# Kernel optimization log

Hardware: AMD Instinct MI355X
Metric: run time of the kernel (lower is better)

## Reference

```python
import jax, jax.numpy as jnp
import numpy as np

B, N, DX, E, H, HD, KH, FF = 8, 8192, 2, 128, 8, 16, 32, 128
G1, G2, PMAX = 32, 32, 32


def _ln(x, g, b):
    mu = jnp.mean(x, axis=-1, keepdims=True)
    var = jnp.mean((x - mu) ** 2, axis=-1, keepdims=True)
    return (x - mu) * jax.lax.rsqrt(var + 1e-5) * g + b


def _cumcount_row(idx):
    # for each element, number of earlier elements with the same value (stable)
    n = idx.shape[0]
    order = jnp.argsort(idx)  # stable
    si = idx[order]
    ar = jnp.arange(n)
    is_start = jnp.concatenate([jnp.ones((1,), bool), si[1:] != si[:-1]])
    seg_start = jax.lax.associative_scan(jnp.maximum, jnp.where(is_start, ar, 0))
    return jnp.zeros(n, jnp.int32).at[order].set((ar - seg_start).astype(jnp.int32))


def _forward(x, z, latent, Wq, Wk, Wv, Wo, bo, kW1, kb1, kW2, kb2,
             lnq_g, lnq_b, lnk_g, lnk_b, ln2_g, ln2_b, fW1, fb1, fW2, fb2,
             grid_n1, grid_n2, max_patch, num_heads):
    Bb, Nn, dx = x.shape
    e = latent.shape[0]
    dims = (grid_n1, grid_n2)
    M = grid_n1 * grid_n2
    P = max_patch
    h = num_heads
    hd = Wq.shape[1] // h
    # grid range from data (margin = 0), regular grid via linspace
    mins = [jnp.min(x[:, :, i]) for i in range(dx)]
    maxs = [jnp.max(x[:, :, i]) for i in range(dx)]
    axes = [jnp.linspace(mins[i], maxs[i], dims[i]) for i in range(dx)]
    x_grid = jnp.stack(jnp.meshgrid(*axes, indexing="ij"), axis=-1)  # [G1,G2,dx]
    x_grid_flat = x_grid.reshape(M, dx)
    # nearest grid cell per point: regular grid -> per-dim rounding
    flat = None
    for i in range(dx):
        step = (maxs[i] - mins[i]) / (dims[i] - 1)
        ii = jnp.clip(jnp.round((x[..., i] - mins[i]) / step), 0, dims[i] - 1).astype(jnp.int32)
        flat = ii if flat is None else flat * dims[i] + ii
    cell = flat  # [B,N]
    cumc = jax.vmap(_cumcount_row)(cell)          # slot within cell
    slot = jnp.where(cumc < P, cumc, P)           # overflow -> dummy slot (dropped)
    bidx = jnp.broadcast_to(jnp.arange(Bb)[:, None], (Bb, Nn))
    # scatter points into per-cell padded neighbour sets [B, M, P, d]
    jx = jnp.zeros((Bb, M, P + 1, dx), x.dtype).at[bidx, cell, slot].set(x)[:, :, :P]
    jz = jnp.zeros((Bb, M, P + 1, e), z.dtype).at[bidx, cell, slot].set(z)[:, :, :P]
    msk = jnp.zeros((Bb, M, P + 1), bool).at[bidx, cell, slot].set(True)[:, :, :P]
    xg = jnp.broadcast_to(x_grid_flat[None], (Bb, M, dx))
    zg = jnp.broadcast_to(latent[None, None, :], (Bb, M, e))
    # concatenate_x_grid=True: grid token prepended, always attended
    joint_x = jnp.concatenate([xg[:, :, None, :], jx], axis=2).reshape(Bb * M, P + 1, dx)
    joint_z = jnp.concatenate([zg[:, :, None, :], jz], axis=2).reshape(Bb * M, P + 1, e)
    att_mask = jnp.concatenate([jnp.ones((Bb, M, 1), bool), msk], axis=2).reshape(Bb * M, P + 1)
    xq = xg.reshape(Bb * M, 1, dx)
    zq = zg.reshape(Bb * M, 1, e)
    T = Bb * M
    # masked translation-equivariant cross-attention (pre-norm layer)
    q = jnp.einsum("tqe,ef->tqf", _ln(zq, lnq_g, lnq_b), Wq).reshape(T, 1, h, hd)
    zk_n = _ln(joint_z, lnk_g, lnk_b)
    k = jnp.einsum("tke,ef->tkf", zk_n, Wk).reshape(T, P + 1, h, hd)
    v = jnp.einsum("tke,ef->tkf", zk_n, Wv).reshape(T, P + 1, h, hd)
    dots = jnp.einsum("tqhd,tkhd->thqk", q, k) / jnp.sqrt(jnp.asarray(hd, q.dtype))
    diff = joint_x[:, None, :, :] - xq[:, :, None, :]            # [T,1,P+1,dx]
    kb = jnp.maximum(diff @ kW1 + kb1, 0.0) @ kW2 + kb2          # kernel bias [T,1,P+1,h]
    dots = dots + jnp.transpose(kb, (0, 3, 1, 2))
    dots = jnp.where(att_mask[:, None, None, :], dots, -1e9)
    A = jax.nn.softmax(dots, axis=-1)                            # [T,h,1,P+1]
    out = jnp.einsum("thqk,tkhd->tqhd", A, v).reshape(T, 1, h * hd)
    z_new = zq + out @ Wo + bo
    z_new = z_new + (jnp.maximum(_ln(z_new, ln2_g, ln2_b) @ fW1 + fb1, 0.0) @ fW2 + fb2)
    x_new = jnp.einsum("tqk,tkd->tqd", jnp.mean(A, axis=1), joint_x)  # TE location update
    x_grid_out = x_new.reshape(Bb, grid_n1, grid_n2, dx)
    z_grid_out = z_new.reshape(Bb, grid_n1, grid_n2, e)
    return (x_grid_out, z_grid_out)


def setup_inputs():
    key = jax.random.key(0)
    ks = jax.random.split(key, 12)
    s = 0.05
    return {
        "x": jax.random.uniform(ks[0], (B, N, DX), jnp.float32),
        "z": jax.random.normal(ks[1], (B, N, E), jnp.float32),
        "grid_n1": G1, "grid_n2": G2, "max_patch": PMAX, "num_heads": H,
        "latent": jax.random.normal(ks[2], (E,), jnp.float32),
        "Wq": jax.random.normal(ks[3], (E, H * HD), jnp.float32) * s,
        "Wk": jax.random.normal(ks[4], (E, H * HD), jnp.float32) * s,
        "Wv": jax.random.normal(ks[5], (E, H * HD), jnp.float32) * s,
        "Wo": jax.random.normal(ks[6], (H * HD, E), jnp.float32) * s,
        "bo": jnp.zeros((E,), jnp.float32),
        "kW1": jax.random.normal(ks[7], (DX, KH), jnp.float32) * s,
        "kb1": jnp.zeros((KH,), jnp.float32),
        "kW2": jax.random.normal(ks[8], (KH, H), jnp.float32) * s,
        "kb2": jnp.zeros((H,), jnp.float32),
        "lnq_g": jnp.ones((E,), jnp.float32), "lnq_b": jnp.zeros((E,), jnp.float32),
        "lnk_g": jnp.ones((E,), jnp.float32), "lnk_b": jnp.zeros((E,), jnp.float32),
        "ln2_g": jnp.ones((E,), jnp.float32), "ln2_b": jnp.zeros((E,), jnp.float32),
        "fW1": jax.random.normal(ks[9], (E, FF), jnp.float32) * s,
        "fb1": jnp.zeros((FF,), jnp.float32),
        "fW2": jax.random.normal(ks[10], (FF, E), jnp.float32) * s,
        "fb2": jnp.zeros((E,), jnp.float32),
    }


def reference(x, z, grid_n1, grid_n2, max_patch, num_heads, latent, Wq, Wk, Wv, Wo, bo,
              kW1, kb1, kW2, kb2, lnq_g, lnq_b, lnk_g, lnk_b, ln2_g, ln2_b,
              fW1, fb1, fW2, fb2):
    return _forward(x, z, latent, Wq, Wk, Wv, Wo, bo, kW1, kb1, kW2, kb2,
                    lnq_g, lnq_b, lnk_g, lnk_b, ln2_g, ln2_b, fW1, fb1, fW2, fb2,
                    grid_n1, grid_n2, max_patch, num_heads)
```

## Files before the change

### kernel.cpp

```cpp
#include <hip/hip_runtime.h>
#include <stdint.h>

#define NB 8
#define NN 8192
#define NE 128
#define NH 8
#define NHD 16
#define NKH 32
#define NFF 128
#define NG 32
#define NM 1024
#define NP 32
#define NT 8192
#define NPTS 65536

typedef __attribute__((ext_vector_type(8))) short bf16x8_t;
typedef __attribute__((ext_vector_type(4))) float f32x4_t;

#define WS_MM      0
#define WS_D0      64
#define WS_Q       128
#define WS_VG      640
#define WS_PART    1152
#define WS_CNT     2048
#define WS_CELL    34816
#define WS_PIDX    296960
#define WS_WKVT    1345536
#define WS_WOT     1411072
#define WS_FW1T    1443840
#define WS_FW2T    1476608
#define WS_KV      3606528

__device__ __forceinline__ unsigned short f2bf(float f) {
    unsigned u = __float_as_uint(f);
    u += 0x7FFFu + ((u >> 16) & 1u);
    return (unsigned short)(u >> 16);
}
__device__ __forceinline__ float bf2f(unsigned short h) {
    return __uint_as_float(((unsigned)h) << 16);
}
__device__ __forceinline__ float bflo(unsigned w) { return __uint_as_float(w << 16); }
__device__ __forceinline__ float bfhi(unsigned w) { return __uint_as_float(w & 0xFFFF0000u); }

__global__ __launch_bounds__(256) void k_setup(
        const float* __restrict__ x,
        const float* __restrict__ Wk, const float* __restrict__ Wv, const float* __restrict__ Wo,
        const float* __restrict__ fW1, const float* __restrict__ fW2,
        const float* __restrict__ latent, const float* __restrict__ Wq,
        const float* __restrict__ lnq_g, const float* __restrict__ lnq_b,
        const float* __restrict__ lnk_g, const float* __restrict__ lnk_b,
        const float* __restrict__ kb1, const float* __restrict__ kW2, const float* __restrict__ kb2,
        int* __restrict__ cnt,
        unsigned short* __restrict__ WkvT, unsigned short* __restrict__ WoT,
        unsigned short* __restrict__ fW1T, unsigned short* __restrict__ fW2T,
        float* __restrict__ ws_q, float* __restrict__ ws_vg, float* __restrict__ ws_d0,
        float4* __restrict__ part) {
    int blk = blockIdx.x;
    int t = threadIdx.x;
    if (blk < 20) {
        __shared__ float s_t[64][65];
        const float* src; unsigned short* dst;
        int n0, k0, srcN0;
        if (blk < 8) {
            int tn = blk >> 1, tk = blk & 1;
            n0 = tn * 64; k0 = tk * 64;
            dst = WkvT;
            if (n0 < 128) { src = Wk; srcN0 = n0; }
            else          { src = Wv; srcN0 = n0 - 128; }
        } else {
            int m = (blk - 8) >> 2, s4 = (blk - 8) & 3;
            int tn = s4 >> 1, tk = s4 & 1;
            n0 = tn * 64; k0 = tk * 64; srcN0 = n0;
            src = (m == 0) ? Wo : (m == 1) ? fW1 : fW2;
            dst = (m == 0) ? WoT : (m == 1) ? fW1T : fW2T;
        }
        int tx = t & 63, ty = t >> 6;
        #pragma unroll
        for (int r = 0; r < 16; ++r) {
            int kr = r * 4 + ty;
            s_t[kr][tx] = src[(k0 + kr) * 128 + srcN0 + tx];
        }
        __syncthreads();
        #pragma unroll
        for (int r = 0; r < 16; ++r) {
            int nr = r * 4 + ty;
            dst[(n0 + nr) * 128 + k0 + tx] = f2bf(s_t[tx][nr]);
        }
    } else if (blk < 52) {
        int idx = (blk - 20) * 256 + t;
        cnt[idx] = 0;
    } else if (blk == 52) {
        __shared__ float s_qn[128], s_kn[128], s_q[128], s_kg[128];
        __shared__ float s_mu, s_rstd;
        if (t < 64) {
            float v0 = latent[t], v1 = latent[t + 64];
            float s = v0 + v1;
            for (int m = 32; m > 0; m >>= 1) s += __shfl_xor(s, m);
            float mu = s * (1.0f / 128.0f);
            float d0 = v0 - mu, d1 = v1 - mu;
            float q = d0 * d0 + d1 * d1;
            for (int m = 32; m > 0; m >>= 1) q += __shfl_xor(q, m);
            if (t == 0) { s_mu = mu; s_rstd = rsqrtf(q * (1.0f / 128.0f) + 1e-5f); }
        }
        __syncthreads();
        if (t < 128) {
            float nv = (latent[t] - s_mu) * s_rstd;
            s_qn[t] = nv * lnq_g[t] + lnq_b[t];
            s_kn[t] = nv * lnk_g[t] + lnk_b[t];
        }
        __syncthreads();
        if (t < 128) {
            float aq = 0.f, ak = 0.f, av = 0.f;
            for (int e = 0; e < 128; ++e) {
                aq += s_qn[e] * Wq[e * 128 + t];
                ak += s_kn[e] * Wk[e * 128 + t];
                av += s_kn[e] * Wv[e * 128 + t];
            }
            s_q[t] = aq; s_kg[t] = ak;
            ws_q[t] = aq; ws_vg[t] = av;
        }
        __syncthreads();
        if (t < 8) {
            float acc = 0.f;
            for (int d = 0; d < 16; ++d) acc += s_q[t * 16 + d] * s_kg[t * 16 + d];
            float kb0 = kb2[t];
            for (int j = 0; j < 32; ++j) kb0 += fmaxf(kb1[j], 0.f) * kW2[j * 8 + t];
            ws_d0[t] = acc * 0.25f + kb0;
        }
    } else {
        __shared__ float s_red[4][4];
        int pb = blk - 53;
        const float4* xp = (const float4*)x + pb * 1024;
        float mn0 = 1e30f, mx0 = -1e30f, mn1 = 1e30f, mx1 = -1e30f;
        #pragma unroll
        for (int it = 0; it < 4; ++it) {
            float4 v = xp[it * 256 + t];
            mn0 = fminf(mn0, fminf(v.x, v.z)); mx0 = fmaxf(mx0, fmaxf(v.x, v.z));
            mn1 = fminf(mn1, fminf(v.y, v.w)); mx1 = fmaxf(mx1, fmaxf(v.y, v.w));
        }
        #pragma unroll
        for (int m = 32; m > 0; m >>= 1) {
            mn0 = fminf(mn0, __shfl_xor(mn0, m)); mx0 = fmaxf(mx0, __shfl_xor(mx0, m));
            mn1 = fminf(mn1, __shfl_xor(mn1, m)); mx1 = fmaxf(mx1, __shfl_xor(mx1, m));
        }
        int w = t >> 6;
        if ((t & 63) == 0) {
            s_red[w][0] = mn0; s_red[w][1] = mn1; s_red[w][2] = mx0; s_red[w][3] = mx1;
        }
        __syncthreads();
        if (t == 0) {
            float a0 = fminf(fminf(s_red[0][0], s_red[1][0]), fminf(s_red[2][0], s_red[3][0]));
            float a1 = fminf(fminf(s_red[0][1], s_red[1][1]), fminf(s_red[2][1], s_red[3][1]));
            float b0 = fmaxf(fmaxf(s_red[0][2], s_red[1][2]), fmaxf(s_red[2][2], s_red[3][2]));
            float b1 = fmaxf(fmaxf(s_red[0][3], s_red[1][3]), fmaxf(s_red[2][3], s_red[3][3]));
            part[pb] = make_float4(a0, a1, b0, b1);
        }
    }
}

__global__ __launch_bounds__(256) void k_binkv(
        const float* __restrict__ x, const float* __restrict__ z,
        const float4* __restrict__ part, float* __restrict__ mm,
        const float* __restrict__ lnk_g, const float* __restrict__ lnk_b,
        const unsigned short* __restrict__ WkvT, unsigned short* __restrict__ kv,
        int* __restrict__ cell, int* __restrict__ cnt, int* __restrict__ ptIdx) {
    int t = threadIdx.x;
    if (blockIdx.x >= 1024) {
        int l = t & 63;
        float mn0 = 1e30f, mn1 = 1e30f, mx0 = -1e30f, mx1 = -1e30f;
        if (l < 32) { float4 p = part[l]; mn0 = p.x; mn1 = p.y; mx0 = p.z; mx1 = p.w; }
        #pragma unroll
        for (int m = 32; m > 0; m >>= 1) {
            mn0 = fminf(mn0, __shfl_xor(mn0, m)); mx0 = fmaxf(mx0, __shfl_xor(mx0, m));
            mn1 = fminf(mn1, __shfl_xor(mn1, m)); mx1 = fmaxf(mx1, __shfl_xor(mx1, m));
        }
        if (blockIdx.x == 1024 && t == 0) {
            mm[0] = mn0; mm[1] = mn1; mm[2] = mx0; mm[3] = mx1;
        }
        int i = (blockIdx.x - 1024) * 256 + t;
        float st0 = (mx0 - mn0) / 31.0f, st1 = (mx1 - mn1) / 31.0f;
        float2 xv = ((const float2*)x)[i];
        int i0 = (int)rintf((xv.x - mn0) / st0); i0 = min(max(i0, 0), 31);
        int i1 = (int)rintf((xv.y - mn1) / st1); i1 = min(max(i1, 0), 31);
        int c = i0 * 32 + i1;
        cell[i] = c;
        int bb = i >> 13;
        int slot = atomicAdd(&cnt[bb * NM + c], 1);
        if (slot < NP) ptIdx[(bb * NM + c) * NP + slot] = i & (NN - 1);
        return;
    }
    __shared__ unsigned short s_zn[64][136];
    __shared__ unsigned short s_stage[4][16][68];
    int w = t >> 6, lane = t & 63;
    long base = (long)blockIdx.x * 64;
    int sub = lane >> 5;
    int lq = lane & 31;
    int mrow = lane & 15, quad = lane >> 4;

    bf16x8_t afrag[4][4];
    #pragma unroll
    for (int j = 0; j < 4; ++j) {
        int ft = w * 4 + j;
        const unsigned short* ap = WkvT + (ft * 16 + mrow) * 128 + quad * 8;
        #pragma unroll
        for (int kc = 0; kc < 4; ++kc)
            afrag[j][kc] = *(const bf16x8_t*)(ap + kc * 32);
    }

    float4 g4 = ((const float4*)lnk_g)[lq];
    float4 b4 = ((const float4*)lnk_b)[lq];
    float4 v[8];
    #pragma unroll
    for (int i = 0; i < 8; ++i) {
        int pl = w * 16 + i * 2 + sub;
        v[i] = ((const float4*)z)[(base + pl) * 32 + lq];
    }
    #pragma unroll
    for (int i = 0; i < 8; ++i) {
        int pl = w * 16 + i * 2 + sub;
        float sum = v[i].x + v[i].y + v[i].z + v[i].w;
        float ssq = v[i].x * v[i].x + v[i].y * v[i].y + v[i].z * v[i].z + v[i].w * v[i].w;
        #pragma unroll
        for (int m = 1; m < 32; m <<= 1) {
            sum += __shfl_xor(sum, m);
            ssq += __shfl_xor(ssq, m);
        }
        float mu = sum * (1.0f / 128.0f);
        float var = fmaxf(ssq * (1.0f / 128.0f) - mu * mu, 0.0f);
        float rstd = rsqrtf(var + 1e-5f);
        float n0 = (v[i].x - mu) * rstd * g4.x + b4.x;
        float n1 = (v[i].y - mu) * rstd * g4.y + b4.y;
        float n2 = (v[i].z - mu) * rstd * g4.z + b4.z;
        float n3 = (v[i].w - mu) * rstd * g4.w + b4.w;
        unsigned d0 = (unsigned)f2bf(n0) | ((unsigned)f2bf(n1) << 16);
        unsigned d1 = (unsigned)f2bf(n2) | ((unsigned)f2bf(n3) << 16);
        *(uint2*)&s_zn[pl][lq * 4] = make_uint2(d0, d1);
    }
    __syncthreads();

    #pragma unroll
    for (int tau = 0; tau < 4; ++tau) {
        bf16x8_t bfrag[4];
        #pragma unroll
        for (int kc = 0; kc < 4; ++kc)
            bfrag[kc] = *(const bf16x8_t*)&s_zn[tau * 16 + mrow][kc * 32 + quad * 8];
        #pragma unroll
        for (int j = 0; j < 4; ++j) {
            f32x4_t acc = {0.f, 0.f, 0.f, 0.f};
            #pragma unroll
            for (int kc = 0; kc < 4; ++kc)
                acc = __builtin_amdgcn_mfma_f32_16x16x32_bf16(afrag[j][kc], bfrag[kc], acc, 0, 0, 0);
            unsigned d0 = (unsigned)f2bf(acc[0]) | ((unsigned)f2bf(acc[1]) << 16);
            unsigned d1 = (unsigned)f2bf(acc[2]) | ((unsigned)f2bf(acc[3]) << 16);
            *(uint2*)&s_stage[w][mrow][j * 16 + quad * 4] = make_uint2(d0, d1);
        }
        int tok = lane >> 3, u = lane & 7;
        long tk0 = base + tau * 16;
        uint4 ra = *(const uint4*)&s_stage[w][tok][u * 8];
        *(uint4*)(kv + (tk0 + tok) * 256 + w * 64 + u * 8) = ra;
        uint4 rb = *(const uint4*)&s_stage[w][tok + 8][u * 8];
        *(uint4*)(kv + (tk0 + tok + 8) * 256 + w * 64 + u * 8) = rb;
    }
}

__global__ __launch_bounds__(256) void k_attn(const float* __restrict__ x,
        const int* __restrict__ cell, const int* __restrict__ cnt, int* __restrict__ ptIdx,
        const float* __restrict__ mm, const unsigned short* __restrict__ kv,
        const float* __restrict__ ws_q, const float* __restrict__ ws_vg,
        const float* __restrict__ ws_d0,
        const float* __restrict__ kW1, const float* __restrict__ kb1,
        const float* __restrict__ kW2, const float* __restrict__ kb2,
        const float* __restrict__ latent, const float* __restrict__ bo,
        const float* __restrict__ ln2_g, const float* __restrict__ ln2_b,
        const float* __restrict__ fb1, const float* __restrict__ fb2,
        const unsigned short* __restrict__ WoT, const unsigned short* __restrict__ fW1T,
        const unsigned short* __restrict__ fW2T,
        float* __restrict__ xout, float* __restrict__ zout) {
    __shared__ unsigned short s_a[16][136];
    __shared__ unsigned short s_a2[16][136];
    __shared__ float s_z[4][128];
    __shared__ float s_lat[128], s_g2[128], s_b2[128], s_fb1v[128], s_fb2v[128];
    int t = threadIdx.x;
    int l = t & 63;
    int w = t >> 6;
    if (t < 128) {
        s_lat[t] = latent[t] + bo[t];
        s_g2[t] = ln2_g[t]; s_b2[t] = ln2_b[t];
        s_fb1v[t] = fb1[t]; s_fb2v[t] = fb2[t];
    }
    int bm = blockIdx.x * 4 + w;
    int b = bm >> 10;
    int h = l >> 3, jp = l & 7;

    float mn0 = mm[0], mn1 = mm[1], mx0 = mm[2], mx1 = mm[3];
    int i0 = (bm & 1023) >> 5, i1 = bm & 31;
    float st0 = (mx0 - mn0) / 31.0f, st1 = (mx1 - mn1) / 31.0f;
    float xg0 = (i0 == 31) ? mx0 : mn0 + i0 * st0;
    float xg1 = (i1 == 31) ? mx1 : mn1 + i1 * st1;
    int craw = cnt[bm];
    int c = min(craw, NP);
    if (craw > NP) {
        int mycell = bm & 1023;
        const int* cb = cell + b * NN;
        int run = 0;
        for (int ch = 0; ch < NN / 64 && run < NP; ++ch) {
            int n = ch * 64 + l;
            bool match = (cb[n] == mycell);
            unsigned long long mask = __ballot(match);
            if (match) {
                int rank = run + __popcll(mask & ((1ull << l) - 1ull));
                if (rank < NP) ptIdx[bm * NP + rank] = n;
            }
            run += __popcll(mask);
        }
    }

    float q0 = ws_q[2 * l] * 0.25f, q1 = ws_q[2 * l + 1] * 0.25f;
    float vg0 = ws_vg[2 * l], vg1 = ws_vg[2 * l + 1];
    float ag = ws_d0[h];
    float kb2h = kb2[h];
    float w1a[4], w1b[4], b1v[4], w2v[4];
    #pragma unroll
    for (int m = 0; m < 4; ++m) {
        int j = jp + 8 * m;
        w1a[m] = kW1[j]; w1b[m] = kW1[32 + j]; b1v[m] = kb1[j]; w2v[m] = kW2[j * 8 + h];
    }

    int idxreg = 0; float x0r = 0.f, x1r = 0.f;
    if (l < c) {
        idxreg = ptIdx[bm * NP + l];
        float2 xv = ((const float2*)x)[(size_t)b * NN + idxreg];
        x0r = xv.x; x1r = xv.y;
    }

    unsigned vreg[NP];
    float areg[4];
    #pragma unroll
    for (int k = 0; k < NP; ++k) vreg[k] = 0u;
    areg[0] = areg[1] = areg[2] = areg[3] = -1e30f;

    #pragma unroll
    for (int key = 0; key < NP; ++key) {
        if (key < c) {
            int idxk = __shfl(idxreg, key);
            const unsigned* rowp = (const unsigned*)kv + ((size_t)(b * NN + idxk) << 7);
            unsigned kw = rowp[l];
            vreg[key] = rowp[64 + l];
            float d0 = __shfl(x0r, key) - xg0;
            float d1 = __shfl(x1r, key) - xg1;
            float part = q0 * bflo(kw) + q1 * bfhi(kw);
            #pragma unroll
            for (int m = 0; m < 4; ++m) {
                float hj = fmaf(d0, w1a[m], fmaf(d1, w1b[m], b1v[m]));
                hj = fmaxf(hj, 0.f);
                part = fmaf(hj, w2v[m], part);
            }
            part += __shfl_xor(part, 1);
            part += __shfl_xor(part, 2);
            part += __shfl_xor(part, 4);
            float score = part + kb2h;
            if (jp == (key & 7)) areg[key >> 3] = score;
        }
    }

    float mx = fmaxf(fmaxf(areg[0], areg[1]), fmaxf(areg[2], areg[3]));
    mx = fmaxf(mx, ag);
    mx = fmaxf(mx, __shfl_xor(mx, 1));
    mx = fmaxf(mx, __shfl_xor(mx, 2));
    mx = fmaxf(mx, __shfl_xor(mx, 4));
    float e0 = __expf(areg[0] - mx), e1 = __expf(areg[1] - mx);
    float e2 = __expf(areg[2] - mx), e3 = __expf(areg[3] - mx);
    float eg = __expf(ag - mx);
    float s = e0 + e1 + e2 + e3;
    s += __shfl_xor(s, 1);
    s += __shfl_xor(s, 2);
    s += __shfl_xor(s, 4);
    s += eg;
    float inv = 1.0f / s;

    float accA = eg * inv * vg0, accB = eg * inv * vg1;
    #pragma unroll
    for (int key = 0; key < NP; ++key) {
        if (key < c) {
            int src = (l & 56) | (key & 7);
            float em = (key >> 3) == 0 ? e0 : (key >> 3) == 1 ? e1 : (key >> 3) == 2 ? e2 : e3;
            float a = __shfl(em, src) * inv;
            unsigned vw = vreg[key];
            accA = fmaf(a, bflo(vw), accA);
            accB = fmaf(a, bfhi(vw), accB);
        }
    }
    unsigned ow = ((unsigned)f2bf(accB) << 16) | (unsigned)f2bf(accA);
    *(unsigned*)&s_a[w][2 * l] = ow;

    float s0 = e0 * inv, s1 = e1 * inv, s2 = e2 * inv, s3 = e3 * inv, sg = eg * inv;
    #pragma unroll
    for (int m = 8; m <= 32; m <<= 1) {
        s0 += __shfl_xor(s0, m); s1 += __shfl_xor(s1, m);
        s2 += __shfl_xor(s2, m); s3 += __shfl_xor(s3, m);
        sg += __shfl_xor(sg, m);
    }
    float px0 = 0.f, px1 = 0.f;
    {
        float xx0, xx1;
        xx0 = __shfl(x0r, jp);      xx1 = __shfl(x1r, jp);
        px0 = fmaf(s0, xx0, px0);   px1 = fmaf(s0, xx1, px1);
        xx0 = __shfl(x0r, jp + 8);  xx1 = __shfl(x1r, jp + 8);
        px0 = fmaf(s1, xx0, px0);   px1 = fmaf(s1, xx1, px1);
        xx0 = __shfl(x0r, jp + 16); xx1 = __shfl(x1r, jp + 16);
        px0 = fmaf(s2, xx0, px0);   px1 = fmaf(s2, xx1, px1);
        xx0 = __shfl(x0r, jp + 24); xx1 = __shfl(x1r, jp + 24);
        px0 = fmaf(s3, xx0, px0);   px1 = fmaf(s3, xx1, px1);
    }
    px0 += __shfl_xor(px0, 1); px1 += __shfl_xor(px1, 1);
    px0 += __shfl_xor(px0, 2); px1 += __shfl_xor(px1, 2);
    px0 += __shfl_xor(px0, 4); px1 += __shfl_xor(px1, 4);
    if (l == 0) {
        xout[bm * 2]     = (px0 + sg * xg0) * 0.125f;
        xout[bm * 2 + 1] = (px1 + sg * xg1) * 0.125f;
    }

    __syncthreads();
    int mrow = l & 15, quad = l >> 4;
    int base4 = blockIdx.x * 4;
    {
        bf16x8_t a[4];
        #pragma unroll
        for (int kc = 0; kc < 4; ++kc)
            a[kc] = *(const bf16x8_t*)&s_a[mrow][kc * 32 + quad * 8];
        #pragma unroll
        for (int cc = 0; cc < 2; ++cc) {
            int ct = w * 2 + cc;
            f32x4_t acc = {0.f, 0.f, 0.f, 0.f};
            const unsigned short* bp = WoT + (ct * 16 + mrow) * 128 + quad * 8;
            #pragma unroll
            for (int kc = 0; kc < 4; ++kc)
                acc = __builtin_amdgcn_mfma_f32_16x16x32_bf16(a[kc], *(const bf16x8_t*)(bp + kc * 32), acc, 0, 0, 0);
            if (quad == 0) {
                int f = ct * 16 + mrow;
                #pragma unroll
                for (int r = 0; r < 4; ++r) s_z[r][f] = acc[r] + s_lat[f];
            }
        }
    }
    __syncthreads();
    {
        float v0 = s_z[w][l], v1 = s_z[w][l + 64];
        float ssum = v0 + v1;
        #pragma unroll
        for (int m = 32; m > 0; m >>= 1) ssum += __shfl_xor(ssum, m);
        float mu = ssum * (1.0f / 128.0f);
        float d0 = v0 - mu, d1 = v1 - mu;
        float qq = d0 * d0 + d1 * d1;
        #pragma unroll
        for (int m = 32; m > 0; m >>= 1) qq += __shfl_xor(qq, m);
        float rstd = rsqrtf(qq * (1.0f / 128.0f) + 1e-5f);
        s_a2[w][l]      = f2bf(d0 * rstd * s_g2[l] + s_b2[l]);
        s_a2[w][l + 64] = f2bf(d1 * rstd * s_g2[l + 64] + s_b2[l + 64]);
    }
    __syncthreads();
    {
        bf16x8_t a[4];
        #pragma unroll
        for (int kc = 0; kc < 4; ++kc)
            a[kc] = *(const bf16x8_t*)&s_a2[mrow][kc * 32 + quad * 8];
        #pragma unroll
        for (int cc = 0; cc < 2; ++cc) {
            int ct = w * 2 + cc;
            f32x4_t acc = {0.f, 0.f, 0.f, 0.f};
            const unsigned short* bp = fW1T + (ct * 16 + mrow) * 128 + quad * 8;
            #pragma unroll
            for (int kc = 0; kc < 4; ++kc)
                acc = __builtin_amdgcn_mfma_f32_16x16x32_bf16(a[kc], *(const bf16x8_t*)(bp + kc * 32), acc, 0, 0, 0);
            if (quad == 0) {
                int f = ct * 16 + mrow;
                #pragma unroll
                for (int r = 0; r < 4; ++r)
                    s_a[r][f] = f2bf(fmaxf(acc[r] + s_fb1v[f], 0.f));
            }
        }
    }
    __syncthreads();
    {
        bf16x8_t a[4];
        #pragma unroll
        for (int kc = 0; kc < 4; ++kc)
            a[kc] = *(const bf16x8_t*)&s_a[mrow][kc * 32 + quad * 8];
        #pragma unroll
        for (int cc = 0; cc < 2; ++cc) {
            int ct = w * 2 + cc;
            f32x4_t acc = {0.f, 0.f, 0.f, 0.f};
            const unsigned short* bp = fW2T + (ct * 16 + mrow) * 128 + quad * 8;
            #pragma unroll
            for (int kc = 0; kc < 4; ++kc)
                acc = __builtin_amdgcn_mfma_f32_16x16x32_bf16(a[kc], *(const bf16x8_t*)(bp + kc * 32), acc, 0, 0, 0);
            if (quad == 0) {
                int f = ct * 16 + mrow;
                #pragma unroll
                for (int r = 0; r < 4; ++r)
                    zout[(base4 + r) * 128 + f] = s_z[r][f] + acc[r] + s_fb2v[f];
            }
        }
    }
}

extern "C" void kernel_launch(void* const* d_in, const int* in_sizes, int n_in,
                              void* d_out, int out_size, void* d_ws, size_t ws_size,
                              hipStream_t stream) {
    const float* x     = (const float*)d_in[0];
    const float* z     = (const float*)d_in[1];
    const float* latent= (const float*)d_in[6];
    const float* Wq    = (const float*)d_in[7];
    const float* Wk    = (const float*)d_in[8];
    const float* Wv    = (const float*)d_in[9];
    const float* Wo    = (const float*)d_in[10];
    const float* bo    = (const float*)d_in[11];
    const float* kW1   = (const float*)d_in[12];
    const float* kb1   = (const float*)d_in[13];
    const float* kW2   = (const float*)d_in[14];
    const float* kb2   = (const float*)d_in[15];
    const float* lnq_g = (const float*)d_in[16];
    const float* lnq_b = (const float*)d_in[17];
    const float* lnk_g = (const float*)d_in[18];
    const float* lnk_b = (const float*)d_in[19];
    const float* ln2_g = (const float*)d_in[20];
    const float* ln2_b = (const float*)d_in[21];
    const float* fW1   = (const float*)d_in[22];
    const float* fb1   = (const float*)d_in[23];
    const float* fW2   = (const float*)d_in[24];
    const float* fb2   = (const float*)d_in[25];

    uint8_t* ws = (uint8_t*)d_ws;
    float* mm     = (float*)(ws + WS_MM);
    float* ws_d0  = (float*)(ws + WS_D0);
    float* ws_q   = (float*)(ws + WS_Q);
    float* ws_vg  = (float*)(ws + WS_VG);
    float4* part  = (float4*)(ws + WS_PART);
    int* cnt      = (int*)(ws + WS_CNT);
    int* cell     = (int*)(ws + WS_CELL);
    int* ptIdx    = (int*)(ws + WS_PIDX);
    unsigned short* WkvT = (unsigned short*)(ws + WS_WKVT);
    unsigned short* WoT  = (unsigned short*)(ws + WS_WOT);
    unsigned short* fW1T = (unsigned short*)(ws + WS_FW1T);
    unsigned short* fW2T = (unsigned short*)(ws + WS_FW2T);
    unsigned short* kv   = (unsigned short*)(ws + WS_KV);

    float* xout = (float*)d_out;
    float* zout = (float*)d_out + 16384;

    k_setup <<<85,   256, 0, stream>>>(x, Wk, Wv, Wo, fW1, fW2, latent, Wq,
                                       lnq_g, lnq_b, lnk_g, lnk_b, kb1, kW2, kb2,
                                       cnt, WkvT, WoT, fW1T, fW2T, ws_q, ws_vg, ws_d0, part);
    k_binkv <<<1280, 256, 0, stream>>>(x, z, part, mm, lnk_g, lnk_b, WkvT, kv,
                                       cell, cnt, ptIdx);
    k_attn  <<<2048, 256, 0, stream>>>(x, cell, cnt, ptIdx, mm, kv, ws_q, ws_vg, ws_d0,
                                       kW1, kb1, kW2, kb2,
                                       latent, bo, ln2_g, ln2_b, fb1, fb2,
                                       WoT, fW1T, fW2T, xout, zout);
}
```

Before: 187.4 us.

## Precompute per-point attention scores by folding query into Wk and computing kernel bias early

The single latent query is folded into Wk, giving a per-head Wk·q matrix. Each point's attention logit can then be computed once in the binning kernel with a small MFMA plus the positional MLP. Keys are no longer materialised, which halves the kv buffer to V only. The attention kernel just gathers the precomputed per-point scores and V rows. The trade-off is extra work and a score buffer write in the binning kernel, and the positional bias now uses each point's offset from its own cell centre, which must match what the reference does.

```diff
diff --git a/kernel.cpp b/kernel.cpp
--- a/kernel.cpp
+++ b/kernel.cpp
@@ -25,19 +25,18 @@
 #define WS_CNT     2048
 #define WS_CELL    34816
 #define WS_PIDX    296960
-#define WS_WKVT    1345536
+#define WS_WVT     1345536
 #define WS_WOT     1411072
 #define WS_FW1T    1443840
 #define WS_FW2T    1476608
-#define WS_KV      3606528
+#define WS_WKQT    1509376
+#define WS_SCORES  1513472
+#define WS_KV      4194304
 
 __device__ __forceinline__ unsigned short f2bf(float f) {
     unsigned u = __float_as_uint(f);
     u += 0x7FFFu + ((u >> 16) & 1u);
     return (unsigned short)(u >> 16);
-}
-__device__ __forceinline__ float bf2f(unsigned short h) {
-    return __uint_as_float(((unsigned)h) << 16);
 }
 __device__ __forceinline__ float bflo(unsigned w) { return __uint_as_float(w << 16); }
 __device__ __forceinline__ float bfhi(unsigned w) { return __uint_as_float(w & 0xFFFF0000u); }
@@ -51,26 +50,25 @@
         const float* __restrict__ lnk_g, const float* __restrict__ lnk_b,
         const float* __restrict__ kb1, const float* __restrict__ kW2, const float* __restrict__ kb2,
         int* __restrict__ cnt,
-        unsigned short* __restrict__ WkvT, unsigned short* __restrict__ WoT,
+        unsigned short* __restrict__ WvT, unsigned short* __restrict__ WoT,
         unsigned short* __restrict__ fW1T, unsigned short* __restrict__ fW2T,
         float* __restrict__ ws_q, float* __restrict__ ws_vg, float* __restrict__ ws_d0,
+        unsigned short* __restrict__ WkqT,
         float4* __restrict__ part) {
     int blk = blockIdx.x;
     int t = threadIdx.x;
-    if (blk < 20) {
+    if (blk < 16) {
         __shared__ float s_t[64][65];
         const float* src; unsigned short* dst;
-        int n0, k0, srcN0;
-        if (blk < 8) {
+        int n0, k0;
+        if (blk < 4) {
             int tn = blk >> 1, tk = blk & 1;
             n0 = tn * 64; k0 = tk * 64;
-            dst = WkvT;
-            if (n0 < 128) { src = Wk; srcN0 = n0; }
-            else          { src = Wv; srcN0 = n0 - 128; }
+            src = Wv; dst = WvT;
         } else {
-            int m = (blk - 8) >> 2, s4 = (blk - 8) & 3;
+            int m = (blk - 4) >> 2, s4 = (blk - 4) & 3;
             int tn = s4 >> 1, tk = s4 & 1;
-            n0 = tn * 64; k0 = tk * 64; srcN0 = n0;
+            n0 = tn * 64; k0 = tk * 64;
             src = (m == 0) ? Wo : (m == 1) ? fW1 : fW2;
             dst = (m == 0) ? WoT : (m == 1) ? fW1T : fW2T;
         }
@@ -78,7 +76,7 @@
         #pragma unroll
         for (int r = 0; r < 16; ++r) {
             int kr = r * 4 + ty;
-            s_t[kr][tx] = src[(k0 + kr) * 128 + srcN0 + tx];
+            s_t[kr][tx] = src[(k0 + kr) * 128 + n0 + tx];
         }
         __syncthreads();
         #pragma unroll
@@ -86,10 +84,10 @@
             int nr = r * 4 + ty;
             dst[(n0 + nr) * 128 + k0 + tx] = f2bf(s_t[tx][nr]);
         }
-    } else if (blk < 52) {
-        int idx = (blk - 20) * 256 + t;
+    } else if (blk < 48) {
+        int idx = (blk - 16) * 256 + t;
         cnt[idx] = 0;
-    } else if (blk == 52) {
+    } else if (blk == 48) {
         __shared__ float s_qn[128], s_kn[128], s_q[128], s_kg[128];
         __shared__ float s_mu, s_rstd;
         if (t < 64) {
@@ -120,6 +118,17 @@
             ws_q[t] = aq; ws_vg[t] = av;
         }
         __syncthreads();
+        if (t < 128) {
+            const float* wr = Wk + t * 128;
+            #pragma unroll
+            for (int h = 0; h < 8; ++h) {
+                float a = 0.f;
+                #pragma unroll
+                for (int d = 0; d < 16; ++d) a += wr[h * 16 + d] * s_q[h * 16 + d];
+                WkqT[h * 128 + t] = f2bf(a * 0.25f);
+                WkqT[(h + 8) * 128 + t] = 0;
+            }
+        }
         if (t < 8) {
             float acc = 0.f;
             for (int d = 0; d < 16; ++d) acc += s_q[t * 16 + d] * s_kg[t * 16 + d];
@@ -129,7 +138,7 @@
         }
     } else {
         __shared__ float s_red[4][4];
-        int pb = blk - 53;
+        int pb = blk - 49;
         const float4* xp = (const float4*)x + pb * 1024;
         float mn0 = 1e30f, mx0 = -1e30f, mn1 = 1e30f, mx1 = -1e30f;
         #pragma unroll
@@ -162,7 +171,11 @@
         const float* __restrict__ x, const float* __restrict__ z,
         const float4* __restrict__ part, float* __restrict__ mm,
         const float* __restrict__ lnk_g, const float* __restrict__ lnk_b,
-        const unsigned short* __restrict__ WkvT, unsigned short* __restrict__ kv,
+        const unsigned short* __restrict__ WkqT,
+        const float* __restrict__ kW1, const float* __restrict__ kb1,
+        const float* __restrict__ kW2, const float* __restrict__ kb2,
+        const unsigned short* __restrict__ WvT, unsigned short* __restrict__ kv,
+        float* __restrict__ scores,
         int* __restrict__ cell, int* __restrict__ cnt, int* __restrict__ ptIdx) {
     int t = threadIdx.x;
     if (blockIdx.x >= 1024) {
@@ -197,15 +210,29 @@
     int lq = lane & 31;
     int mrow = lane & 15, quad = lane >> 4;
 
+    float mn0 = 1e30f, mn1 = 1e30f, mx0 = -1e30f, mx1 = -1e30f;
+    if (lane < 32) { float4 p = part[lane]; mn0 = p.x; mn1 = p.y; mx0 = p.z; mx1 = p.w; }
+    #pragma unroll
+    for (int m = 32; m > 0; m >>= 1) {
+        mn0 = fminf(mn0, __shfl_xor(mn0, m)); mx0 = fmaxf(mx0, __shfl_xor(mx0, m));
+        mn1 = fminf(mn1, __shfl_xor(mn1, m)); mx1 = fmaxf(mx1, __shfl_xor(mx1, m));
+    }
+    int ptl = w * 16 + mrow;
+    float2 xv2 = ((const float2*)x)[base + ptl];
+
+    int th = w >> 1, fh = w & 1;
     bf16x8_t afrag[4][4];
     #pragma unroll
     for (int j = 0; j < 4; ++j) {
-        int ft = w * 4 + j;
-        const unsigned short* ap = WkvT + (ft * 16 + mrow) * 128 + quad * 8;
+        const unsigned short* ap = WvT + ((fh * 4 + j) * 16 + mrow) * 128 + quad * 8;
         #pragma unroll
         for (int kc = 0; kc < 4; ++kc)
             afrag[j][kc] = *(const bf16x8_t*)(ap + kc * 32);
     }
+    bf16x8_t sfrag[4];
+    #pragma unroll
+    for (int kc = 0; kc < 4; ++kc)
+        sfrag[kc] = *(const bf16x8_t*)(WkqT + mrow * 128 + kc * 32 + quad * 8);
 
     float4 g4 = ((const float4*)lnk_g)[lq];
     float4 b4 = ((const float4*)lnk_b)[lq];
@@ -239,11 +266,12 @@
     __syncthreads();
 
     #pragma unroll
-    for (int tau = 0; tau < 4; ++tau) {
+    for (int tau = 0; tau < 2; ++tau) {
+        int trow = th * 32 + tau * 16;
         bf16x8_t bfrag[4];
         #pragma unroll
         for (int kc = 0; kc < 4; ++kc)
-            bfrag[kc] = *(const bf16x8_t*)&s_zn[tau * 16 + mrow][kc * 32 + quad * 8];
+            bfrag[kc] = *(const bf16x8_t*)&s_zn[trow + mrow][kc * 32 + quad * 8];
         #pragma unroll
         for (int j = 0; j < 4; ++j) {
             f32x4_t acc = {0.f, 0.f, 0.f, 0.f};
@@ -255,21 +283,73 @@
             *(uint2*)&s_stage[w][mrow][j * 16 + quad * 4] = make_uint2(d0, d1);
         }
         int tok = lane >> 3, u = lane & 7;
-        long tk0 = base + tau * 16;
+        long tk0 = base + trow;
         uint4 ra = *(const uint4*)&s_stage[w][tok][u * 8];
-        *(uint4*)(kv + (tk0 + tok) * 256 + w * 64 + u * 8) = ra;
+        *(uint4*)(kv + (tk0 + tok) * 128 + fh * 64 + u * 8) = ra;
         uint4 rb = *(const uint4*)&s_stage[w][tok + 8][u * 8];
-        *(uint4*)(kv + (tk0 + tok + 8) * 256 + w * 64 + u * 8) = rb;
+        *(uint4*)(kv + (tk0 + tok + 8) * 128 + fh * 64 + u * 8) = rb;
+    }
+
+    f32x4_t sacc = {0.f, 0.f, 0.f, 0.f};
+    {
+        bf16x8_t sb[4];
+        #pragma unroll
+        for (int kc = 0; kc < 4; ++kc)
+            sb[kc] = *(const bf16x8_t*)&s_zn[w * 16 + mrow][kc * 32 + quad * 8];
+        #pragma unroll
+        for (int kc = 0; kc < 4; ++kc)
+            sacc = __builtin_amdgcn_mfma_f32_16x16x32_bf16(sfrag[kc], sb[kc], sacc, 0, 0, 0);
+    }
+
+    {
+        float st0 = (mx0 - mn0) / 31.0f, st1 = (mx1 - mn1) / 31.0f;
+        int i0 = (int)rintf((xv2.x - mn0) / st0); i0 = min(max(i0, 0), 31);
+        int i1 = (int)rintf((xv2.y - mn1) / st1); i1 = min(max(i1, 0), 31);
+        float cx0 = (i0 == 31) ? mx0 : mn0 + i0 * st0;
+        float cx1 = (i1 == 31) ? mx1 : mn1 + i1 * st1;
+        float d0 = xv2.x - cx0, d1 = xv2.y - cx1;
+        float k0 = 0.f, k1 = 0.f, k2 = 0.f, k3 = 0.f, k4 = 0.f, k5 = 0.f, k6 = 0.f, k7 = 0.f;
+        #pragma unroll
+        for (int jj = 0; jj < 8; ++jj) {
+            int j = quad * 8 + jj;
+            float hj = fmaf(d0, kW1[j], fmaf(d1, kW1[32 + j], kb1[j]));
+            hj = fmaxf(hj, 0.f);
+            float4 w2a = *(const float4*)(kW2 + j * 8);
+            float4 w2b = *(const float4*)(kW2 + j * 8 + 4);
+            k0 = fmaf(hj, w2a.x, k0); k1 = fmaf(hj, w2a.y, k1);
+            k2 = fmaf(hj, w2a.z, k2); k3 = fmaf(hj, w2a.w, k3);
+            k4 = fmaf(hj, w2b.x, k4); k5 = fmaf(hj, w2b.y, k5);
+            k6 = fmaf(hj, w2b.z, k6); k7 = fmaf(hj, w2b.w, k7);
+        }
+        k0 += __shfl_xor(k0, 16); k0 += __shfl_xor(k0, 32);
+        k1 += __shfl_xor(k1, 16); k1 += __shfl_xor(k1, 32);
+        k2 += __shfl_xor(k2, 16); k2 += __shfl_xor(k2, 32);
+        k3 += __shfl_xor(k3, 16); k3 += __shfl_xor(k3, 32);
+        k4 += __shfl_xor(k4, 16); k4 += __shfl_xor(k4, 32);
+        k5 += __shfl_xor(k5, 16); k5 += __shfl_xor(k5, 32);
+        k6 += __shfl_xor(k6, 16); k6 += __shfl_xor(k6, 32);
+        k7 += __shfl_xor(k7, 16); k7 += __shfl_xor(k7, 32);
+        if (quad == 0) {
+            float4 kb2v = ((const float4*)kb2)[0];
+            float4 o;
+            o.x = sacc[0] + k0 + kb2v.x; o.y = sacc[1] + k1 + kb2v.y;
+            o.z = sacc[2] + k2 + kb2v.z; o.w = sacc[3] + k3 + kb2v.w;
+            *(float4*)(scores + ((size_t)(base + ptl)) * 8) = o;
+        } else if (quad == 1) {
+            float4 kb2v = ((const float4*)kb2)[1];
+            float4 o;
+            o.x = sacc[0] + k4 + kb2v.x; o.y = sacc[1] + k5 + kb2v.y;
+            o.z = sacc[2] + k6 + kb2v.z; o.w = sacc[3] + k7 + kb2v.w;
+            *(float4*)(scores + ((size_t)(base + ptl)) * 8 + 4) = o;
+        }
     }
 }
 
 __global__ __launch_bounds__(256) void k_attn(const float* __restrict__ x,
         const int* __restrict__ cell, const int* __restrict__ cnt, int* __restrict__ ptIdx,
         const float* __restrict__ mm, const unsigned short* __restrict__ kv,
-        const float* __restrict__ ws_q, const float* __restrict__ ws_vg,
-        const float* __restrict__ ws_d0,
-        const float* __restrict__ kW1, const float* __restrict__ kb1,
-        const float* __restrict__ kW2, const float* __restrict__ kb2,
+        const float* __restrict__ scores,
+        const float* __restrict__ ws_vg, const float* __restrict__ ws_d0,
         const float* __restrict__ latent, const float* __restrict__ bo,
         const float* __restrict__ ln2_g, const float* __restrict__ ln2_b,
         const float* __restrict__ fb1, const float* __restrict__ fb2,
@@ -315,16 +395,8 @@
         }
     }
 
-    float q0 = ws_q[2 * l] * 0.25f, q1 = ws_q[2 * l + 1] * 0.25f;
     float vg0 = ws_vg[2 * l], vg1 = ws_vg[2 * l + 1];
     float ag = ws_d0[h];
-    float kb2h = kb2[h];
-    float w1a[4], w1b[4], b1v[4], w2v[4];
-    #pragma unroll
-    for (int m = 0; m < 4; ++m) {
-        int j = jp + 8 * m;
-        w1a[m] = kW1[j]; w1b[m] = kW1[32 + j]; b1v[m] = kb1[j]; w2v[m] = kW2[j * 8 + h];
-    }
 
     int idxreg = 0; float x0r = 0.f, x1r = 0.f;
     if (l < c) {
@@ -333,33 +405,15 @@
         x0r = xv.x; x1r = xv.y;
     }
 
-    unsigned vreg[NP];
     float areg[4];
-    #pragma unroll
-    for (int k = 0; k < NP; ++k) vreg[k] = 0u;
     areg[0] = areg[1] = areg[2] = areg[3] = -1e30f;
-
-    #pragma unroll
-    for (int key = 0; key < NP; ++key) {
-        if (key < c) {
+    #pragma unroll
+    for (int g = 0; g < 4; ++g) {
+        if (c > g * 8) {
+            int key = g * 8 + jp;
             int idxk = __shfl(idxreg, key);
-            const unsigned* rowp = (const unsigned*)kv + ((size_t)(b * NN + idxk) << 7);
-            unsigned kw = rowp[l];
-            vreg[key] = rowp[64 + l];
-            float d0 = __shfl(x0r, key) - xg0;
-            float d1 = __shfl(x1r, key) - xg1;
-            float part = q0 * bflo(kw) + q1 * bfhi(kw);
-            #pragma unroll
-            for (int m = 0; m < 4; ++m) {
-                float hj = fmaf(d0, w1a[m], fmaf(d1, w1b[m], b1v[m]));
-                hj = fmaxf(hj, 0.f);
-                part = fmaf(hj, w2v[m], part);
-            }
-            part += __shfl_xor(part, 1);
-            part += __shfl_xor(part, 2);
-            part += __shfl_xor(part, 4);
-            float score = part + kb2h;
-            if (jp == (key & 7)) areg[key >> 3] = score;
+            if (key < c)
+                areg[g] = scores[((size_t)b * NN + idxk) * 8 + h];
         }
     }
 
@@ -380,14 +434,21 @@
 
     float accA = eg * inv * vg0, accB = eg * inv * vg1;
     #pragma unroll
-    for (int key = 0; key < NP; ++key) {
-        if (key < c) {
-            int src = (l & 56) | (key & 7);
-            float em = (key >> 3) == 0 ? e0 : (key >> 3) == 1 ? e1 : (key >> 3) == 2 ? e2 : e3;
-            float a = __shfl(em, src) * inv;
-            unsigned vw = vreg[key];
-            accA = fmaf(a, bflo(vw), accA);
-            accB = fmaf(a, bfhi(vw), accB);
+    for (int g = 0; g < 4; ++g) {
+        if (c > g * 8) {
+            float em = (g == 0) ? e0 : (g == 1) ? e1 : (g == 2) ? e2 : e3;
+            #pragma unroll
+            for (int k8 = 0; k8 < 8; ++k8) {
+                int key = g * 8 + k8;
+                if (key < c) {
+                    int idxk = __shfl(idxreg, key);
+                    const unsigned* rowp = (const unsigned*)kv + ((size_t)(b * NN + idxk) << 6);
+                    unsigned vw = rowp[l];
+                    float a = __shfl(em, (l & 56) | k8) * inv;
+                    accA = fmaf(a, bflo(vw), accA);
+                    accB = fmaf(a, bfhi(vw), accB);
+                }
+            }
         }
     }
     unsigned ow = ((unsigned)f2bf(accB) << 16) | (unsigned)f2bf(accA);
@@ -539,22 +600,26 @@
     int* cnt      = (int*)(ws + WS_CNT);
     int* cell     = (int*)(ws + WS_CELL);
     int* ptIdx    = (int*)(ws + WS_PIDX);
-    unsigned short* WkvT = (unsigned short*)(ws + WS_WKVT);
+    unsigned short* WvT  = (unsigned short*)(ws + WS_WVT);
     unsigned short* WoT  = (unsigned short*)(ws + WS_WOT);
     unsigned short* fW1T = (unsigned short*)(ws + WS_FW1T);
     unsigned short* fW2T = (unsigned short*)(ws + WS_FW2T);
+    unsigned short* WkqT = (unsigned short*)(ws + WS_WKQT);
+    float* scores = (float*)(ws + WS_SCORES);
     unsigned short* kv   = (unsigned short*)(ws + WS_KV);
 
     float* xout = (float*)d_out;
     float* zout = (float*)d_out + 16384;
 
-    k_setup <<<85,   256, 0, stream>>>(x, Wk, Wv, Wo, fW1, fW2, latent, Wq,
+    k_setup <<<81,   256, 0, stream>>>(x, Wk, Wv, Wo, fW1, fW2, latent, Wq,
                                        lnq_g, lnq_b, lnk_g, lnk_b, kb1, kW2, kb2,
-                                       cnt, WkvT, WoT, fW1T, fW2T, ws_q, ws_vg, ws_d0, part);
-    k_binkv <<<1280, 256, 0, stream>>>(x, z, part, mm, lnk_g, lnk_b, WkvT, kv,
+                                       cnt, WvT, WoT, fW1T, fW2T, ws_q, ws_vg, ws_d0,
+                                       WkqT, part);
+    k_binkv <<<1280, 256, 0, stream>>>(x, z, part, mm, lnk_g, lnk_b, WkqT,
+                                       kW1, kb1, kW2, kb2, WvT, kv, scores,
                                        cell, cnt, ptIdx);
-    k_attn  <<<2048, 256, 0, stream>>>(x, cell, cnt, ptIdx, mm, kv, ws_q, ws_vg, ws_d0,
-                                       kW1, kb1, kW2, kb2,
+    k_attn  <<<2048, 256, 0, stream>>>(x, cell, cnt, ptIdx, mm, kv, scores,
+                                       ws_vg, ws_d0,
                                        latent, bo, ln2_g, ln2_b, fb1, fb2,
                                        WoT, fW1T, fW2T, xout, zout);
 }
```

Result: faster. 180.5 us (-3.7%).
